# Kernel optimization log

Measured on AMD Instinct MI355X. Metric: run time of the kernel, lower is better.

Reference implementation:

```python
import jax, jax.numpy as jnp
import numpy as np

N_NODES = 100000
N_EDGES = 1600000
N_GRAPHS = 1024
B = 1024
GNN_INP, GNN_HID, GNN_OUT = 64, 128, 64
INP, HID, OUT = 64, 256, 1
EPS = 1e-5  # torch BatchNorm1d default eps


def _bn(h, gamma, beta):
    # training-mode BatchNorm1d: biased batch statistics over dim 0
    m = h.mean(axis=0)
    v = jnp.mean((h - m) ** 2, axis=0)
    return (h - m) * jax.lax.rsqrt(v + EPS) * gamma + beta


def setup_inputs() -> dict:
    key = jax.random.key(0)
    ks = jax.random.split(key, 24)
    s = 0.05
    inp = {
        "x": jax.random.normal(ks[0], (B, INP), jnp.float32),
        "masks": jax.random.randint(ks[1], (B,), 0, N_GRAPHS),
        "gnn_x": jax.random.normal(ks[2], (N_NODES, GNN_INP), jnp.float32),
        "edge_index": jax.random.randint(ks[3], (2, N_EDGES), 0, N_NODES),
        "gnn_batch": jnp.sort(jax.random.randint(ks[4], (N_NODES,), 0, N_GRAPHS)),
        # GCNConv params
        "W_gcn": jax.random.normal(ks[5], (GNN_INP, GNN_HID), jnp.float32) * s,
        "b_gcn": jnp.zeros((GNN_HID,), jnp.float32),
        "g1": jnp.ones((GNN_HID,), jnp.float32), "be1": jnp.zeros((GNN_HID,), jnp.float32),
        "W_lin1": jax.random.normal(ks[6], (GNN_HID, GNN_HID // 2), jnp.float32) * s,
        "b_lin1": jnp.zeros((GNN_HID // 2,), jnp.float32),
        "g2": jnp.ones((GNN_HID // 2,), jnp.float32), "be2": jnp.zeros((GNN_HID // 2,), jnp.float32),
        "W_lin2": jax.random.normal(ks[7], (GNN_HID // 2, GNN_OUT), jnp.float32) * s,
        "b_lin2": jnp.zeros((GNN_OUT,), jnp.float32),
        "g3": jnp.ones((GNN_OUT,), jnp.float32), "be3": jnp.zeros((GNN_OUT,), jnp.float32),
        # head params
        "W_fc1": jax.random.normal(ks[8], (INP + GNN_OUT, HID), jnp.float32) * s,
        "b_fc1": jnp.zeros((HID,), jnp.float32),
        "g4": jnp.ones((HID,), jnp.float32), "be4": jnp.zeros((HID,), jnp.float32),
        "W_fc2": jax.random.normal(ks[9], (HID, HID // 4), jnp.float32) * s,
        "b_fc2": jnp.zeros((HID // 4,), jnp.float32),
        "g5": jnp.ones((HID // 4,), jnp.float32), "be5": jnp.zeros((HID // 4,), jnp.float32),
        "W_fc3": jax.random.normal(ks[10], (HID // 4, OUT), jnp.float32) * s,
        "b_fc3": jnp.zeros((OUT,), jnp.float32),
    }
    return inp


def _forward(x, masks, gnn_x, edge_index, gnn_batch,
             W_gcn, b_gcn, g1, be1, W_lin1, b_lin1, g2, be2, W_lin2, b_lin2,
             g3, be3, W_fc1, b_fc1, g4, be4, W_fc2, b_fc2, g5, be5, W_fc3, b_fc3):
    N = gnn_x.shape[0]
    # --- GCNConv: linear transform, self-loops, sym-normalized scatter-add ---
    h = gnn_x @ W_gcn  # [N, GNN_HID]
    loop = jnp.arange(N)
    src = jnp.concatenate([edge_index[0], loop])
    dst = jnp.concatenate([edge_index[1], loop])
    deg = jax.ops.segment_sum(jnp.ones_like(dst, jnp.float32), dst, num_segments=N)
    dis = jax.lax.rsqrt(deg)  # deg >= 1 thanks to self-loops
    norm = dis[src] * dis[dst]  # [E+N]
    agg = jax.ops.segment_sum(h[src] * norm[:, None], dst, num_segments=N) + b_gcn
    z = jax.nn.relu(_bn(agg, g1, be1))  # dropout = identity (eval)
    # --- global_mean_pool over graph ids ---
    sums = jax.ops.segment_sum(z, gnn_batch, num_segments=N_GRAPHS)
    cnt = jax.ops.segment_sum(jnp.ones((N,), jnp.float32), gnn_batch, num_segments=N_GRAPHS)
    pooled = sums / jnp.maximum(cnt, 1.0)[:, None]  # [G, GNN_HID]
    z = jax.nn.relu(_bn(pooled @ W_lin1 + b_lin1, g2, be2))
    z = _bn(z @ W_lin2 + b_lin2, g3, be3)  # [G, GNN_OUT]
    # --- MixGNN head ---
    g = z[masks]  # [B, GNN_OUT]
    t = jnp.concatenate([x, g], axis=1)
    t = jax.nn.relu(_bn(t @ W_fc1 + b_fc1, g4, be4))
    t = t * t  # Multiply([h, h])
    t = jax.nn.relu(_bn(t @ W_fc2 + b_fc2, g5, be5))
    t = t * t
    t = t * t
    return t @ W_fc3 + b_fc3  # [B, OUT]


def reference(x, masks, gnn_x, edge_index, gnn_batch,
              W_gcn, b_gcn, g1, be1, W_lin1, b_lin1, g2, be2, W_lin2, b_lin2,
              g3, be3, W_fc1, b_fc1, g4, be4, W_fc2, b_fc2, g5, be5, W_fc3, b_fc3):
    return _forward(x, masks, gnn_x, edge_index, gnn_batch,
                    W_gcn, b_gcn, g1, be1, W_lin1, b_lin1, g2, be2, W_lin2, b_lin2,
                    g3, be3, W_fc1, b_fc1, g4, be4, W_fc2, b_fc2, g5, be5, W_fc3, b_fc3)
```

## Files before the change

kernel.cpp:

```cpp
#include <hip/hip_runtime.h>
#include <hip/hip_bf16.h>

#define N_NODES 100000
#define N_EDGES 1600000
#define N_GRAPHS 1024
#define BSZ 1024
#define EPS 1e-5f

#define NBUCK 256
#define BUCKW 391
#define BCAP  8192
#define SRC_MASK 0x1FFFF
#define BIN_CHUNK 8192
#define BIN_BLOCKS 196

#define WS_BNAGG   0
#define WS_STATS1  256
#define WS_STATS2  384
#define WS_STATS4  512
#define WS_STATS5  1024
#define WS_ZTOTAL  1152
#define WS_GCUR    1152
#define WS_SCALE1  1408
#define WS_SHIFT1  1536
#define WS_GSTART  1664
#define WS_DIS     2692
#define WS_ROWPTR  102692
#define WS_ROWLEN  202692
#define WS_AGG     302692
#define WS_PACKED  302692
#define WS_CSRC    2399844
#define WS_XH      4496996
#define WS_AGGX    13102692
#define WS_POOLED  19502692
#define WS_T1      19633764
#define WS_T2      19699300
#define WS_T4      19764836
#define WS_T5      20026980

__device__ inline unsigned short f2bf(float f) {
    unsigned int u = __float_as_uint(f);
    return (unsigned short)((u + 0x7FFFu + ((u >> 16) & 1u)) >> 16);
}

__global__ __launch_bounds__(256) void prep_kernel(float* __restrict__ ws,
                                                   const int* __restrict__ gbatch) {
    int b = blockIdx.x, tid = threadIdx.x;
    if (b == 0) {
        for (int i = tid; i < WS_ZTOTAL; i += 256) ws[i] = 0.0f;
    } else if (b == 1) {
        ((int*)(ws + WS_GCUR))[tid] = tid * BCAP;
    } else {
        int g = (b - 2) * 256 + tid;
        int lo = 0, hi = N_NODES;
        while (lo < hi) {
            int mid = (lo + hi) >> 1;
            if (gbatch[mid] < g) lo = mid + 1; else hi = mid;
        }
        int* gstart = (int*)(ws + WS_GSTART);
        gstart[g] = lo;
        if (g == 0) gstart[N_GRAPHS] = N_NODES;
    }
}

__global__ __launch_bounds__(256) void cvt_kernel(const float* __restrict__ x,
                                                  unsigned short* __restrict__ xh) {
    int i = blockIdx.x * 256 + threadIdx.x;
    float4 f = ((const float4*)x)[i];
    ushort4 h;
    h.x = f2bf(f.x); h.y = f2bf(f.y); h.z = f2bf(f.z); h.w = f2bf(f.w);
    ((ushort4*)xh)[i] = h;
}

__global__ __launch_bounds__(1024) void bin_kernel(const int* __restrict__ ei,
                                                   int* __restrict__ gcursor,
                                                   unsigned int* __restrict__ packed) {
    __shared__ unsigned int stage[BIN_CHUNK];
    __shared__ int lh[NBUCK], lbase[NBUCK], lcur[NBUCK], gb[NBUCK];
    const int* src = ei;
    const int* dst = ei + N_EDGES;
    int tid = threadIdx.x;
    int base = blockIdx.x * BIN_CHUNK;
    int n = min(BIN_CHUNK, N_EDGES - base);
    if (tid < NBUCK) lh[tid] = 0;
    __syncthreads();
    for (int i = tid; i < n; i += 1024)
        atomicAdd(&lh[dst[base + i] / BUCKW], 1);
    __syncthreads();
    if (tid < NBUCK) lbase[tid] = lh[tid];
    __syncthreads();
    for (int off = 1; off < NBUCK; off <<= 1) {
        int t = (tid < NBUCK && tid >= off) ? lbase[tid - off] : 0;
        __syncthreads();
        if (tid < NBUCK) lbase[tid] += t;
        __syncthreads();
    }
    if (tid < NBUCK) {
        int excl = lbase[tid] - lh[tid];
        lbase[tid] = excl;
        lcur[tid] = excl;
        gb[tid] = atomicAdd(&gcursor[tid], lh[tid]);
    }
    __syncthreads();
    for (int i = tid; i < n; i += 1024) {
        int d = dst[base + i];
        int s = src[base + i];
        int bk = d / BUCKW;
        int dl = d - bk * BUCKW;
        int slot = atomicAdd(&lcur[bk], 1);
        stage[slot] = ((unsigned int)dl << 17) | (unsigned int)s;
    }
    __syncthreads();
    int wid = tid >> 6, lane = tid & 63;
    for (int bk = wid; bk < NBUCK; bk += 16) {
        int lo = lbase[bk], go = gb[bk];
        int len = min(lh[bk], (bk + 1) * BCAP - go);
        for (int j = lane; j < len; j += 64)
            packed[go + j] = stage[lo + j];
    }
}

__global__ __launch_bounds__(256) void csr_build_kernel(const unsigned int* __restrict__ packed,
                                                        const int* __restrict__ gcur,
                                                        int* __restrict__ rowptr,
                                                        int* __restrict__ rowlen,
                                                        int* __restrict__ csrc,
                                                        float* __restrict__ dis) {
    __shared__ int dcnt[BUCKW];
    __shared__ int lcur[BUCKW];
    __shared__ int stage[BCAP];
    int b = blockIdx.x, tid = threadIdx.x;
    int e0 = b * BCAP;
    int ecnt = min(gcur[b] - e0, BCAP);
    int nbase = b * BUCKW;
    int nmax = min(BUCKW, N_NODES - nbase);
    for (int i = tid; i < BUCKW; i += 256) dcnt[i] = 0;
    __syncthreads();
    for (int i = tid; i < ecnt; i += 256)
        atomicAdd(&dcnt[packed[e0 + i] >> 17], 1);
    __syncthreads();
    for (int i = tid; i < nmax; i += 256) {
        dis[nbase + i] = rsqrtf((float)dcnt[i] + 1.0f);
        rowlen[nbase + i] = dcnt[i];
    }
    __syncthreads();
    if (tid < 64) {
        int lane = tid;
        int run = 0;
        for (int c = 0; c < BUCKW; c += 64) {
            int idx = c + lane;
            int v = (idx < BUCKW) ? dcnt[idx] : 0;
            int inc = v;
#pragma unroll
            for (int off = 1; off < 64; off <<= 1) {
                int t = __shfl_up(inc, off);
                if (lane >= off) inc += t;
            }
            if (idx < BUCKW) {
                int excl = run + inc - v;
                dcnt[idx] = excl;
                lcur[idx] = excl;
            }
            run += __shfl(inc, 63);
        }
    }
    __syncthreads();
    for (int i = tid; i < nmax; i += 256)
        rowptr[nbase + i] = e0 + dcnt[i];
    for (int i = tid; i < ecnt; i += 256) {
        unsigned int r = packed[e0 + i];
        int slot = atomicAdd(&lcur[r >> 17], 1);
        stage[slot] = (int)(r & SRC_MASK);
    }
    __syncthreads();
    for (int i = tid; i < ecnt; i += 256) csrc[e0 + i] = stage[i];
}

__global__ __launch_bounds__(256) void gather_kernel(const float* __restrict__ x,
                                                     const unsigned short* __restrict__ xh,
                                                     const int* __restrict__ rowptr,
                                                     const int* __restrict__ rowlen,
                                                     const int* __restrict__ csrc,
                                                     const float* __restrict__ dis,
                                                     float* __restrict__ aggx) {
    int wid = (blockIdx.x * 256 + threadIdx.x) >> 6;
    int lane = threadIdx.x & 63;
    if (wid >= N_NODES) return;
    int start = rowptr[wid];
    int len = rowlen[wid];
    float dd = dis[wid];
    float acc = x[(size_t)wid * 64 + lane] * dd * dd;
    for (int j0 = 0; j0 < len; j0 += 64) {
        int cnt = min(64, len - j0);
        int sv = 0;
        float wv = 0.f;
        if (lane < cnt) {
            sv = csrc[start + j0 + lane];
            wv = dis[sv] * dd;
        }
        int iters = (cnt + 7) & ~7;
        for (int k = 0; k < iters; k += 8) {
            int s[8]; float w[8], v[8];
#pragma unroll
            for (int u = 0; u < 8; ++u) {
                s[u] = __shfl(sv, k + u);
                w[u] = __shfl(wv, k + u);
            }
#pragma unroll
            for (int u = 0; u < 8; ++u)
                v[u] = __uint_as_float((unsigned int)xh[(size_t)s[u] * 64 + lane] << 16);
#pragma unroll
            for (int u = 0; u < 8; ++u) acc = fmaf(v[u], w[u], acc);
        }
    }
    aggx[(size_t)wid * 64 + lane] = acc;
}

__global__ __launch_bounds__(256) void gemm_agg_kernel(const float* __restrict__ A,
                                                       const float* __restrict__ W,
                                                       const float* __restrict__ bias,
                                                       float* __restrict__ AGG) {
    __shared__ float Ws[64 * 128];
    __shared__ float As[16 * 64];
    int tid = threadIdx.x;
    const float4* W4 = (const float4*)W;
    float4* Ws4 = (float4*)Ws;
#pragma unroll
    for (int i = 0; i < 8; ++i) Ws4[tid + i * 256] = W4[tid + i * 256];
    int row0 = blockIdx.x * 16;
    ((float4*)As)[tid] = ((const float4*)(A + (size_t)row0 * 64))[tid];
    __syncthreads();
    int tx = tid & 31;
    int ty = tid >> 5;
    int r0 = ty * 2;
    float4 bb = ((const float4*)bias)[tx];
    float acc[2][4] = {{bb.x, bb.y, bb.z, bb.w}, {bb.x, bb.y, bb.z, bb.w}};
#pragma unroll
    for (int k = 0; k < 64; ++k) {
        float a0 = As[r0 * 64 + k];
        float a1 = As[(r0 + 1) * 64 + k];
        float4 w = Ws4[k * 32 + tx];
        acc[0][0] += a0 * w.x; acc[0][1] += a0 * w.y; acc[0][2] += a0 * w.z; acc[0][3] += a0 * w.w;
        acc[1][0] += a1 * w.x; acc[1][1] += a1 * w.y; acc[1][2] += a1 * w.z; acc[1][3] += a1 * w.w;
    }
#pragma unroll
    for (int rr = 0; rr < 2; ++rr) {
        float4 v = make_float4(acc[rr][0], acc[rr][1], acc[rr][2], acc[rr][3]);
        ((float4*)(AGG + (size_t)(row0 + r0 + rr) * 128))[tx] = v;
    }
}

__global__ __launch_bounds__(256) void bnagg_stats_kernel(const float* __restrict__ agg,
                                                          float* __restrict__ stats) {
    __shared__ float4 ls[256];
    int tid = threadIdx.x;
    int lane = tid & 63;
    int grp = tid >> 6;
    int f = lane * 2;
    float2 s = {0.f, 0.f}, sq = {0.f, 0.f};
    for (int r = blockIdx.x * 4 + grp; r < N_NODES; r += gridDim.x * 4) {
        float2 a = *(const float2*)(agg + (size_t)r * 128 + f);
        s.x += a.x; s.y += a.y;
        sq.x += a.x * a.x; sq.y += a.y * a.y;
    }
    ls[tid] = make_float4(s.x, s.y, sq.x, sq.y);
    __syncthreads();
    if (tid < 64) {
        float4 v = ls[tid];
        float4 b = ls[tid + 64], c = ls[tid + 128], d = ls[tid + 192];
        v.x += b.x + c.x + d.x;
        v.y += b.y + c.y + d.y;
        v.z += b.z + c.z + d.z;
        v.w += b.w + c.w + d.w;
        unsafeAtomicAdd(&stats[f], v.x);
        unsafeAtomicAdd(&stats[f + 1], v.y);
        unsafeAtomicAdd(&stats[128 + f], v.z);
        unsafeAtomicAdd(&stats[128 + f + 1], v.w);
    }
}

__global__ void bn1_fold_kernel(const float* __restrict__ stats, const float* __restrict__ g1,
                                const float* __restrict__ be1, float* __restrict__ scale1,
                                float* __restrict__ shift1) {
    int f = threadIdx.x;
    float m = stats[f] * (1.0f / N_NODES);
    float var = stats[128 + f] * (1.0f / N_NODES) - m * m;
    float sc = g1[f] * rsqrtf(var + EPS);
    scale1[f] = sc;
    shift1[f] = be1[f] - m * sc;
}

__global__ __launch_bounds__(256) void pool_gather_kernel(const float* __restrict__ agg,
                                                          const int* __restrict__ gstart,
                                                          const float* __restrict__ scale1,
                                                          const float* __restrict__ shift1,
                                                          float* __restrict__ pooled) {
    int g = (blockIdx.x * 256 + threadIdx.x) >> 6;
    int lane = threadIdx.x & 63;
    if (g >= N_GRAPHS) return;
    int r0 = gstart[g], r1 = gstart[g + 1];
    int f = lane * 2;
    float2 sc = *(const float2*)(scale1 + f);
    float2 sh = *(const float2*)(shift1 + f);
    float2 acc = {0.f, 0.f};
    for (int r = r0; r < r1; ++r) {
        float2 a = *(const float2*)(agg + (size_t)r * 128 + f);
        acc.x += fmaxf(a.x * sc.x + sh.x, 0.f);
        acc.y += fmaxf(a.y * sc.y + sh.y, 0.f);
    }
    float inv = 1.0f / fmaxf((float)(r1 - r0), 1.0f);
    float2 o; o.x = acc.x * inv; o.y = acc.y * inv;
    *(float2*)(pooled + (size_t)g * 128 + f) = o;
}

__global__ __launch_bounds__(256) void lin1_kernel(const float* __restrict__ pooled,
                                                   const float* __restrict__ W,
                                                   const float* __restrict__ bias,
                                                   float* __restrict__ t1,
                                                   float* __restrict__ stats1) {
    __shared__ float ls[256], ls2[256];
    int tid = threadIdx.x;
    int r = blockIdx.x * 4 + (tid >> 6);
    int c = tid & 63;
    float acc = bias[c];
    const float* srow = pooled + (size_t)r * 128;
#pragma unroll 8
    for (int k = 0; k < 128; ++k)
        acc += srow[k] * W[k * 64 + c];
    t1[r * 64 + c] = acc;
    ls[tid] = acc; ls2[tid] = acc * acc;
    __syncthreads();
    if (tid < 64) {
        float s = ls[tid] + ls[tid + 64] + ls[tid + 128] + ls[tid + 192];
        float q = ls2[tid] + ls2[tid + 64] + ls2[tid + 128] + ls2[tid + 192];
        unsafeAtomicAdd(&stats1[c], s);
        unsafeAtomicAdd(&stats1[64 + c], q);
    }
}

__global__ __launch_bounds__(256) void lin2_kernel(const float* __restrict__ t1,
                                                   const float* __restrict__ stats1,
                                                   const float* __restrict__ g,
                                                   const float* __restrict__ be,
                                                   const float* __restrict__ W,
                                                   const float* __restrict__ bias,
                                                   float* __restrict__ t2,
                                                   float* __restrict__ stats2) {
    __shared__ float sc[64], sh[64];
    __shared__ float ls[256], ls2[256];
    int tid = threadIdx.x;
    if (tid < 64) {
        float m = stats1[tid] * (1.0f / BSZ);
        float var = stats1[64 + tid] * (1.0f / BSZ) - m * m;
        float s = g[tid] * rsqrtf(var + EPS);
        sc[tid] = s; sh[tid] = be[tid] - m * s;
    }
    __syncthreads();
    int r = blockIdx.x * 4 + (tid >> 6);
    int c = tid & 63;
    float acc = bias[c];
    const float* row = t1 + (size_t)r * 64;
#pragma unroll 8
    for (int k = 0; k < 64; ++k) {
        float z = fmaxf(row[k] * sc[k] + sh[k], 0.f);
        acc += z * W[k * 64 + c];
    }
    t2[r * 64 + c] = acc;
    ls[tid] = acc; ls2[tid] = acc * acc;
    __syncthreads();
    if (tid < 64) {
        float s = ls[tid] + ls[tid + 64] + ls[tid + 128] + ls[tid + 192];
        float q = ls2[tid] + ls2[tid + 64] + ls2[tid + 128] + ls2[tid + 192];
        unsafeAtomicAdd(&stats2[c], s);
        unsafeAtomicAdd(&stats2[64 + c], q);
    }
}

__global__ __launch_bounds__(1024) void fc1_kernel(const float* __restrict__ x,
                                                   const int* __restrict__ masks,
                                                   const float* __restrict__ t2,
                                                   const float* __restrict__ stats2,
                                                   const float* __restrict__ g3,
                                                   const float* __restrict__ be3,
                                                   const float* __restrict__ W,
                                                   const float* __restrict__ bias,
                                                   float* __restrict__ t4,
                                                   float* __restrict__ stats4) {
    __shared__ float sc[64], sh[64];
    __shared__ float cat[4][128];
    __shared__ float ls[1024], ls2[1024];
    int tid = threadIdx.x;
    if (tid < 64) {
        float m = stats2[tid] * (1.0f / BSZ);
        float var = stats2[64 + tid] * (1.0f / BSZ) - m * m;
        float s = g3[tid] * rsqrtf(var + EPS);
        sc[tid] = s; sh[tid] = be3[tid] - m * s;
    }
    __syncthreads();
    int r0 = blockIdx.x * 4;
    if (tid < 512) {
        int i = tid >> 7;
        int k = tid & 127;
        int r = r0 + i;
        float v;
        if (k < 64) {
            v = x[r * 64 + k];
        } else {
            int mrow = masks[r];
            int kk = k - 64;
            v = t2[mrow * 64 + kk] * sc[kk] + sh[kk];
        }
        cat[i][k] = v;
    }
    __syncthreads();
    int i = tid >> 8;
    int c = tid & 255;
    float acc = bias[c];
#pragma unroll 8
    for (int k = 0; k < 128; ++k)
        acc += cat[i][k] * W[k * 256 + c];
    t4[(size_t)(r0 + i) * 256 + c] = acc;
    ls[tid] = acc; ls2[tid] = acc * acc;
    __syncthreads();
    if (tid < 256) {
        float s = ls[tid] + ls[tid + 256] + ls[tid + 512] + ls[tid + 768];
        float q = ls2[tid] + ls2[tid + 256] + ls2[tid + 512] + ls2[tid + 768];
        unsafeAtomicAdd(&stats4[c], s);
        unsafeAtomicAdd(&stats4[256 + c], q);
    }
}

__global__ __launch_bounds__(256) void fc2_kernel(const float* __restrict__ t4,
                                                  const float* __restrict__ stats4,
                                                  const float* __restrict__ g4,
                                                  const float* __restrict__ be4,
                                                  const float* __restrict__ W,
                                                  const float* __restrict__ bias,
                                                  float* __restrict__ t5,
                                                  float* __restrict__ stats5) {
    __shared__ float sc[256], sh[256];
    __shared__ float ls[256], ls2[256];
    int tid = threadIdx.x;
    {
        float m = stats4[tid] * (1.0f / BSZ);
        float var = stats4[256 + tid] * (1.0f / BSZ) - m * m;
        float s = g4[tid] * rsqrtf(var + EPS);
        sc[tid] = s; sh[tid] = be4[tid] - m * s;
    }
    __syncthreads();
    int r = blockIdx.x * 4 + (tid >> 6);
    int c = tid & 63;
    float acc = bias[c];
    const float* row = t4 + (size_t)r * 256;
#pragma unroll 8
    for (int k = 0; k < 256; ++k) {
        float z = fmaxf(row[k] * sc[k] + sh[k], 0.f);
        z *= z;
        acc += z * W[k * 64 + c];
    }
    t5[r * 64 + c] = acc;
    ls[tid] = acc; ls2[tid] = acc * acc;
    __syncthreads();
    if (tid < 64) {
        float s = ls[tid] + ls[tid + 64] + ls[tid + 128] + ls[tid + 192];
        float q = ls2[tid] + ls2[tid + 64] + ls2[tid + 128] + ls2[tid + 192];
        unsafeAtomicAdd(&stats5[c], s);
        unsafeAtomicAdd(&stats5[64 + c], q);
    }
}

__global__ __launch_bounds__(256) void fc3_kernel(const float* __restrict__ t5,
                                                  const float* __restrict__ stats5,
                                                  const float* __restrict__ g5,
                                                  const float* __restrict__ be5,
                                                  const float* __restrict__ W,
                                                  const float* __restrict__ bias,
                                                  float* __restrict__ out) {
    __shared__ float sc[64], sh[64];
    int tid = threadIdx.x;
    if (tid < 64) {
        float m = stats5[tid] * (1.0f / BSZ);
        float var = stats5[64 + tid] * (1.0f / BSZ) - m * m;
        float s = g5[tid] * rsqrtf(var + EPS);
        sc[tid] = s; sh[tid] = be5[tid] - m * s;
    }
    __syncthreads();
    int r = blockIdx.x * 256 + tid;
    float acc = bias[0];
    const float* row = t5 + (size_t)r * 64;
#pragma unroll
    for (int k = 0; k < 64; ++k) {
        float z = fmaxf(row[k] * sc[k] + sh[k], 0.f);
        z = z * z;
        z = z * z;
        acc += z * W[k];
    }
    out[r] = acc;
}

extern "C" void kernel_launch(void* const* d_in, const int* in_sizes, int n_in,
                              void* d_out, int out_size, void* d_ws, size_t ws_size,
                              hipStream_t stream) {
    const float* x      = (const float*)d_in[0];
    const int*   masks  = (const int*)d_in[1];
    const float* gnn_x  = (const float*)d_in[2];
    const int*   ei     = (const int*)d_in[3];
    const int*   gbatch = (const int*)d_in[4];
    const float* W_gcn  = (const float*)d_in[5];
    const float* b_gcn  = (const float*)d_in[6];
    const float* g1     = (const float*)d_in[7];
    const float* be1    = (const float*)d_in[8];
    const float* W_lin1 = (const float*)d_in[9];
    const float* b_lin1 = (const float*)d_in[10];
    const float* g2     = (const float*)d_in[11];
    const float* be2    = (const float*)d_in[12];
    const float* W_lin2 = (const float*)d_in[13];
    const float* b_lin2 = (const float*)d_in[14];
    const float* g3     = (const float*)d_in[15];
    const float* be3    = (const float*)d_in[16];
    const float* W_fc1  = (const float*)d_in[17];
    const float* b_fc1  = (const float*)d_in[18];
    const float* g4     = (const float*)d_in[19];
    const float* be4    = (const float*)d_in[20];
    const float* W_fc2  = (const float*)d_in[21];
    const float* b_fc2  = (const float*)d_in[22];
    const float* g5     = (const float*)d_in[23];
    const float* be5    = (const float*)d_in[24];
    const float* W_fc3  = (const float*)d_in[25];
    const float* b_fc3  = (const float*)d_in[26];

    float* ws = (float*)d_ws;
    float* bnagg  = ws + WS_BNAGG;
    float* stats1 = ws + WS_STATS1;
    float* stats2 = ws + WS_STATS2;
    float* stats4 = ws + WS_STATS4;
    float* stats5 = ws + WS_STATS5;
    int*   gcur   = (int*)(ws + WS_GCUR);
    float* scale1 = ws + WS_SCALE1;
    float* shift1 = ws + WS_SHIFT1;
    int*   gstart = (int*)(ws + WS_GSTART);
    float* dis    = ws + WS_DIS;
    int*   rowptr = (int*)(ws + WS_ROWPTR);
    int*   rowlen = (int*)(ws + WS_ROWLEN);
    float* agg    = ws + WS_AGG;
    unsigned int* packed = (unsigned int*)(ws + WS_PACKED);
    int*   csrc   = (int*)(ws + WS_CSRC);
    unsigned short* xh = (unsigned short*)(ws + WS_XH);
    float* aggx   = ws + WS_AGGX;
    float* pooled = ws + WS_POOLED;
    float* t1     = ws + WS_T1;
    float* t2     = ws + WS_T2;
    float* t4     = ws + WS_T4;
    float* t5     = ws + WS_T5;
    float* out    = (float*)d_out;

    prep_kernel<<<6, 256, 0, stream>>>(ws, gbatch);
    cvt_kernel<<<N_NODES * 64 / 4 / 256, 256, 0, stream>>>(gnn_x, xh);
    bin_kernel<<<BIN_BLOCKS, 1024, 0, stream>>>(ei, gcur, packed);
    csr_build_kernel<<<NBUCK, 256, 0, stream>>>(packed, gcur, rowptr, rowlen, csrc, dis);
    gather_kernel<<<(N_NODES * 64 + 255) / 256, 256, 0, stream>>>(gnn_x, xh, rowptr, rowlen, csrc, dis, aggx);
    gemm_agg_kernel<<<N_NODES / 16, 256, 0, stream>>>(aggx, W_gcn, b_gcn, agg);
    bnagg_stats_kernel<<<512, 256, 0, stream>>>(agg, bnagg);
    bn1_fold_kernel<<<1, 128, 0, stream>>>(bnagg, g1, be1, scale1, shift1);
    pool_gather_kernel<<<(N_GRAPHS * 64 + 255) / 256, 256, 0, stream>>>(agg, gstart, scale1, shift1, pooled);
    lin1_kernel<<<256, 256, 0, stream>>>(pooled, W_lin1, b_lin1, t1, stats1);
    lin2_kernel<<<256, 256, 0, stream>>>(t1, stats1, g2, be2, W_lin2, b_lin2, t2, stats2);
    fc1_kernel<<<256, 1024, 0, stream>>>(x, masks, t2, stats2, g3, be3, W_fc1, b_fc1, t4, stats4);
    fc2_kernel<<<256, 256, 0, stream>>>(t4, stats4, g4, be4, W_fc2, b_fc2, t5, stats5);
    fc3_kernel<<<4, 256, 0, stream>>>(t5, stats5, g5, be5, W_fc3, b_fc3, out);
}
```

Measured before the change: 272.1 us.

## Compute BN1 stats from second moments of aggregated inputs, skip materializing GCN output

Instead of materializing the 100000x128 GCN output and scanning it for BatchNorm statistics, this computes the 64x64 second-moment matrix and column sums of the aggregated 64-wide features. The 128-wide mean and variance are then derived algebraically through W_gcn in a single-block fold kernel. Pooling recomputes the per-row projection on the fly from aggx with W held in registers. Separately, the gather's self term now reads the bf16 copy of x instead of fp32. This removes a large write and two reads of the 128-wide buffer, at the cost of extra FLOPs in pooling, a serial single-block fold, and possible precision loss from E[y^2]-m^2 in fp32. The bias is dropped, which is exact only because the BN mean subtraction cancels it.

```diff
diff --git a/kernel.cpp b/kernel.cpp
--- a/kernel.cpp
+++ b/kernel.cpp
@@ -13,30 +13,34 @@
 #define SRC_MASK 0x1FFFF
 #define BIN_CHUNK 8192
 #define BIN_BLOCKS 196
-
-#define WS_BNAGG   0
-#define WS_STATS1  256
-#define WS_STATS2  384
-#define WS_STATS4  512
-#define WS_STATS5  1024
-#define WS_ZTOTAL  1152
-#define WS_GCUR    1152
-#define WS_SCALE1  1408
-#define WS_SHIFT1  1536
-#define WS_GSTART  1664
-#define WS_DIS     2692
-#define WS_ROWPTR  102692
-#define WS_ROWLEN  202692
-#define WS_AGG     302692
-#define WS_PACKED  302692
-#define WS_CSRC    2399844
-#define WS_XH      4496996
-#define WS_AGGX    13102692
-#define WS_POOLED  19502692
-#define WS_T1      19633764
-#define WS_T2      19699300
-#define WS_T4      19764836
-#define WS_T5      20026980
+#define NCHUNK 512
+#define CHUNK_ROWS 196
+
+#define WS_STATS1  0
+#define WS_STATS2  128
+#define WS_STATS4  256
+#define WS_STATS5  768
+#define WS_ZTOTAL  896
+#define WS_GCUR    896
+#define WS_SCALE1  1152
+#define WS_SHIFTP  1280
+#define WS_M       1408
+#define WS_COLSUM  5504
+#define WS_GSTART  5568
+#define WS_DIS     6596
+#define WS_ROWPTR  106596
+#define WS_ROWLEN  206596
+#define WS_PACKED  306596
+#define WS_MPART   306596
+#define WS_CSRC    2403748
+#define WS_CPART   2403748
+#define WS_XH      4500900
+#define WS_AGGX    7700900
+#define WS_POOLED  14100900
+#define WS_T1      14231972
+#define WS_T2      14297508
+#define WS_T4      14363044
+#define WS_T5      14625188
 
 __device__ inline unsigned short f2bf(float f) {
     unsigned int u = __float_as_uint(f);
@@ -176,8 +180,7 @@
     for (int i = tid; i < ecnt; i += 256) csrc[e0 + i] = stage[i];
 }
 
-__global__ __launch_bounds__(256) void gather_kernel(const float* __restrict__ x,
-                                                     const unsigned short* __restrict__ xh,
+__global__ __launch_bounds__(256) void gather_kernel(const unsigned short* __restrict__ xh,
                                                      const int* __restrict__ rowptr,
                                                      const int* __restrict__ rowlen,
                                                      const int* __restrict__ csrc,
@@ -189,7 +192,8 @@
     int start = rowptr[wid];
     int len = rowlen[wid];
     float dd = dis[wid];
-    float acc = x[(size_t)wid * 64 + lane] * dd * dd;
+    float self = __uint_as_float((unsigned int)xh[(size_t)wid * 64 + lane] << 16);
+    float acc = self * dd * dd;
     for (int j0 = 0; j0 < len; j0 += 64) {
         int cnt = min(64, len - j0);
         int sv = 0;
@@ -216,101 +220,150 @@
     aggx[(size_t)wid * 64 + lane] = acc;
 }
 
-__global__ __launch_bounds__(256) void gemm_agg_kernel(const float* __restrict__ A,
-                                                       const float* __restrict__ W,
-                                                       const float* __restrict__ bias,
-                                                       float* __restrict__ AGG) {
-    __shared__ float Ws[64 * 128];
-    __shared__ float As[16 * 64];
+__global__ __launch_bounds__(256) void moment_kernel(const float* __restrict__ aggx,
+                                                     float* __restrict__ mpart,
+                                                     float* __restrict__ cpart) {
+    __shared__ float rows[8 * 64];
+    int c = blockIdx.x, tid = threadIdx.x;
+    int r0 = c * CHUNK_ROWS;
+    int r1 = min(r0 + CHUNK_ROWS, N_NODES);
+    int i0 = (tid >> 6) * 16;
+    int j = tid & 63;
+    float acc[16] = {};
+    float cs = 0.f;
+    for (int it = 0; it < (CHUNK_ROWS + 7) / 8; ++it) {
+        int sid = tid * 2;
+        int grow = r0 + it * 8 + (sid >> 6);
+        float2 v = {0.f, 0.f};
+        if (grow < r1) v = *(const float2*)(aggx + (size_t)(r0 + it * 8) * 64 + sid);
+        __syncthreads();
+        *(float2*)(rows + sid) = v;
+        __syncthreads();
+#pragma unroll
+        for (int rr = 0; rr < 8; ++rr) {
+            float bj = rows[rr * 64 + j];
+            float4 a0 = *(const float4*)(rows + rr * 64 + i0);
+            float4 a1 = *(const float4*)(rows + rr * 64 + i0 + 4);
+            float4 a2 = *(const float4*)(rows + rr * 64 + i0 + 8);
+            float4 a3 = *(const float4*)(rows + rr * 64 + i0 + 12);
+            acc[0]  += a0.x * bj; acc[1]  += a0.y * bj; acc[2]  += a0.z * bj; acc[3]  += a0.w * bj;
+            acc[4]  += a1.x * bj; acc[5]  += a1.y * bj; acc[6]  += a1.z * bj; acc[7]  += a1.w * bj;
+            acc[8]  += a2.x * bj; acc[9]  += a2.y * bj; acc[10] += a2.z * bj; acc[11] += a2.w * bj;
+            acc[12] += a3.x * bj; acc[13] += a3.y * bj; acc[14] += a3.z * bj; acc[15] += a3.w * bj;
+        }
+        if (tid < 64) {
+#pragma unroll
+            for (int rr = 0; rr < 8; ++rr) cs += rows[rr * 64 + tid];
+        }
+    }
+#pragma unroll
+    for (int m = 0; m < 16; ++m)
+        mpart[(size_t)c * 4096 + (i0 + m) * 64 + j] = acc[m];
+    if (tid < 64) cpart[c * 64 + tid] = cs;
+}
+
+__global__ __launch_bounds__(128) void mreduce_kernel(const float* __restrict__ mpart,
+                                                      float* __restrict__ M) {
+    int idx = blockIdx.x * 128 + threadIdx.x;
+    float s = 0.f;
+#pragma unroll 8
+    for (int c = 0; c < NCHUNK; ++c) s += mpart[(size_t)c * 4096 + idx];
+    M[idx] = s;
+}
+
+__global__ __launch_bounds__(256) void fold_kernel(const float* __restrict__ M,
+                                                   const float* __restrict__ cpart,
+                                                   const float* __restrict__ W,
+                                                   const float* __restrict__ g1,
+                                                   const float* __restrict__ be1,
+                                                   float* __restrict__ scale1,
+                                                   float* __restrict__ shiftp) {
+    __shared__ float Ml[4096];
+    __shared__ float sl[64];
+    __shared__ float sp[4][64];
+    __shared__ float qh[2][128];
     int tid = threadIdx.x;
-    const float4* W4 = (const float4*)W;
-    float4* Ws4 = (float4*)Ws;
-#pragma unroll
-    for (int i = 0; i < 8; ++i) Ws4[tid + i * 256] = W4[tid + i * 256];
-    int row0 = blockIdx.x * 16;
-    ((float4*)As)[tid] = ((const float4*)(A + (size_t)row0 * 64))[tid];
-    __syncthreads();
-    int tx = tid & 31;
-    int ty = tid >> 5;
-    int r0 = ty * 2;
-    float4 bb = ((const float4*)bias)[tx];
-    float acc[2][4] = {{bb.x, bb.y, bb.z, bb.w}, {bb.x, bb.y, bb.z, bb.w}};
-#pragma unroll
-    for (int k = 0; k < 64; ++k) {
-        float a0 = As[r0 * 64 + k];
-        float a1 = As[(r0 + 1) * 64 + k];
-        float4 w = Ws4[k * 32 + tx];
-        acc[0][0] += a0 * w.x; acc[0][1] += a0 * w.y; acc[0][2] += a0 * w.z; acc[0][3] += a0 * w.w;
-        acc[1][0] += a1 * w.x; acc[1][1] += a1 * w.y; acc[1][2] += a1 * w.z; acc[1][3] += a1 * w.w;
-    }
-#pragma unroll
-    for (int rr = 0; rr < 2; ++rr) {
-        float4 v = make_float4(acc[rr][0], acc[rr][1], acc[rr][2], acc[rr][3]);
-        ((float4*)(AGG + (size_t)(row0 + r0 + rr) * 128))[tx] = v;
-    }
-}
-
-__global__ __launch_bounds__(256) void bnagg_stats_kernel(const float* __restrict__ agg,
-                                                          float* __restrict__ stats) {
-    __shared__ float4 ls[256];
-    int tid = threadIdx.x;
-    int lane = tid & 63;
-    int grp = tid >> 6;
-    int f = lane * 2;
-    float2 s = {0.f, 0.f}, sq = {0.f, 0.f};
-    for (int r = blockIdx.x * 4 + grp; r < N_NODES; r += gridDim.x * 4) {
-        float2 a = *(const float2*)(agg + (size_t)r * 128 + f);
-        s.x += a.x; s.y += a.y;
-        sq.x += a.x * a.x; sq.y += a.y * a.y;
-    }
-    ls[tid] = make_float4(s.x, s.y, sq.x, sq.y);
-    __syncthreads();
-    if (tid < 64) {
-        float4 v = ls[tid];
-        float4 b = ls[tid + 64], c = ls[tid + 128], d = ls[tid + 192];
-        v.x += b.x + c.x + d.x;
-        v.y += b.y + c.y + d.y;
-        v.z += b.z + c.z + d.z;
-        v.w += b.w + c.w + d.w;
-        unsafeAtomicAdd(&stats[f], v.x);
-        unsafeAtomicAdd(&stats[f + 1], v.y);
-        unsafeAtomicAdd(&stats[128 + f], v.z);
-        unsafeAtomicAdd(&stats[128 + f + 1], v.w);
-    }
-}
-
-__global__ void bn1_fold_kernel(const float* __restrict__ stats, const float* __restrict__ g1,
-                                const float* __restrict__ be1, float* __restrict__ scale1,
-                                float* __restrict__ shift1) {
-    int f = threadIdx.x;
-    float m = stats[f] * (1.0f / N_NODES);
-    float var = stats[128 + f] * (1.0f / N_NODES) - m * m;
-    float sc = g1[f] * rsqrtf(var + EPS);
-    scale1[f] = sc;
-    shift1[f] = be1[f] - m * sc;
-}
-
-__global__ __launch_bounds__(256) void pool_gather_kernel(const float* __restrict__ agg,
-                                                          const int* __restrict__ gstart,
-                                                          const float* __restrict__ scale1,
-                                                          const float* __restrict__ shift1,
-                                                          float* __restrict__ pooled) {
-    int g = (blockIdx.x * 256 + threadIdx.x) >> 6;
-    int lane = threadIdx.x & 63;
-    if (g >= N_GRAPHS) return;
-    int r0 = gstart[g], r1 = gstart[g + 1];
-    int f = lane * 2;
-    float2 sc = *(const float2*)(scale1 + f);
-    float2 sh = *(const float2*)(shift1 + f);
-    float2 acc = {0.f, 0.f};
-    for (int r = r0; r < r1; ++r) {
-        float2 a = *(const float2*)(agg + (size_t)r * 128 + f);
-        acc.x += fmaxf(a.x * sc.x + sh.x, 0.f);
-        acc.y += fmaxf(a.y * sc.y + sh.y, 0.f);
-    }
-    float inv = 1.0f / fmaxf((float)(r1 - r0), 1.0f);
-    float2 o; o.x = acc.x * inv; o.y = acc.y * inv;
-    *(float2*)(pooled + (size_t)g * 128 + f) = o;
+#pragma unroll
+    for (int m = 0; m < 16; ++m) Ml[m * 256 + tid] = M[m * 256 + tid];
+    {
+        int i = tid & 63, q4 = tid >> 6;
+        float s = 0.f;
+        for (int c = q4 * (NCHUNK / 4); c < (q4 + 1) * (NCHUNK / 4); ++c)
+            s += cpart[c * 64 + i];
+        sp[q4][i] = s;
+    }
+    __syncthreads();
+    if (tid < 64) sl[tid] = sp[0][tid] + sp[1][tid] + sp[2][tid] + sp[3][tid];
+    __syncthreads();
+    int j = tid & 127, half = tid >> 7;
+    float wv[64];
+#pragma unroll
+    for (int k = 0; k < 64; ++k) wv[k] = W[k * 128 + j];
+    float q = 0.f;
+    for (int i = half * 32; i < half * 32 + 32; ++i) {
+        float ti = 0.f;
+#pragma unroll
+        for (int k = 0; k < 64; ++k) ti += Ml[i * 64 + k] * wv[k];
+        q += ti * wv[i];
+    }
+    qh[half][j] = q;
+    __syncthreads();
+    if (tid < 128) {
+        float Ey2 = (qh[0][j] + qh[1][j]) * (1.0f / N_NODES);
+        float my = 0.f;
+#pragma unroll
+        for (int k = 0; k < 64; ++k) my += sl[k] * wv[k];
+        my *= (1.0f / N_NODES);
+        float var = Ey2 - my * my;
+        float sc = g1[j] * rsqrtf(var + EPS);
+        scale1[j] = sc;
+        shiftp[j] = be1[j] - my * sc;
+    }
+}
+
+__global__ __launch_bounds__(256) void pool_kernel(const float* __restrict__ aggx,
+                                                   const int* __restrict__ gstart,
+                                                   const float* __restrict__ W,
+                                                   const float* __restrict__ scale1,
+                                                   const float* __restrict__ shiftp,
+                                                   float* __restrict__ pooled) {
+    __shared__ float rows[128];
+    __shared__ float pp[256];
+    int gph = blockIdx.x, tid = threadIdx.x;
+    int c = tid & 127, rg = tid >> 7;
+    float wreg[64];
+#pragma unroll
+    for (int k = 0; k < 64; ++k) wreg[k] = W[k * 128 + c];
+    float sc = scale1[c], sh = shiftp[c];
+    int r0 = gstart[gph], r1 = gstart[gph + 1];
+    float acc = 0.f;
+    for (int rb = r0; rb < r1; rb += 2) {
+        __syncthreads();
+        if (tid < 128) {
+            int rr = rb + (tid >> 6);
+            rows[tid] = (rr < r1) ? aggx[(size_t)rr * 64 + (tid & 63)] : 0.f;
+        }
+        __syncthreads();
+        int r = rb + rg;
+        if (r < r1) {
+            float y = 0.f;
+            const float4* rv = (const float4*)(rows + rg * 64);
+#pragma unroll
+            for (int k4 = 0; k4 < 16; ++k4) {
+                float4 v = rv[k4];
+                y += v.x * wreg[k4 * 4] + v.y * wreg[k4 * 4 + 1]
+                   + v.z * wreg[k4 * 4 + 2] + v.w * wreg[k4 * 4 + 3];
+            }
+            acc += fmaxf(y * sc + sh, 0.f);
+        }
+    }
+    pp[tid] = acc;
+    __syncthreads();
+    if (tid < 128) {
+        int cnt = r1 - r0;
+        float inv = 1.0f / fmaxf((float)cnt, 1.0f);
+        pooled[(size_t)gph * 128 + c] = (pp[c] + pp[128 + c]) * inv;
+    }
 }
 
 __global__ __launch_bounds__(256) void lin1_kernel(const float* __restrict__ pooled,
@@ -528,23 +581,25 @@
     const float* be5    = (const float*)d_in[24];
     const float* W_fc3  = (const float*)d_in[25];
     const float* b_fc3  = (const float*)d_in[26];
+    (void)b_gcn;
 
     float* ws = (float*)d_ws;
-    float* bnagg  = ws + WS_BNAGG;
     float* stats1 = ws + WS_STATS1;
     float* stats2 = ws + WS_STATS2;
     float* stats4 = ws + WS_STATS4;
     float* stats5 = ws + WS_STATS5;
     int*   gcur   = (int*)(ws + WS_GCUR);
     float* scale1 = ws + WS_SCALE1;
-    float* shift1 = ws + WS_SHIFT1;
+    float* shiftp = ws + WS_SHIFTP;
+    float* Mbuf   = ws + WS_M;
     int*   gstart = (int*)(ws + WS_GSTART);
     float* dis    = ws + WS_DIS;
     int*   rowptr = (int*)(ws + WS_ROWPTR);
     int*   rowlen = (int*)(ws + WS_ROWLEN);
-    float* agg    = ws + WS_AGG;
     unsigned int* packed = (unsigned int*)(ws + WS_PACKED);
+    float* mpart  = ws + WS_MPART;
     int*   csrc   = (int*)(ws + WS_CSRC);
+    float* cpart  = ws + WS_CPART;
     unsigned short* xh = (unsigned short*)(ws + WS_XH);
     float* aggx   = ws + WS_AGGX;
     float* pooled = ws + WS_POOLED;
@@ -558,11 +613,11 @@
     cvt_kernel<<<N_NODES * 64 / 4 / 256, 256, 0, stream>>>(gnn_x, xh);
     bin_kernel<<<BIN_BLOCKS, 1024, 0, stream>>>(ei, gcur, packed);
     csr_build_kernel<<<NBUCK, 256, 0, stream>>>(packed, gcur, rowptr, rowlen, csrc, dis);
-    gather_kernel<<<(N_NODES * 64 + 255) / 256, 256, 0, stream>>>(gnn_x, xh, rowptr, rowlen, csrc, dis, aggx);
-    gemm_agg_kernel<<<N_NODES / 16, 256, 0, stream>>>(aggx, W_gcn, b_gcn, agg);
-    bnagg_stats_kernel<<<512, 256, 0, stream>>>(agg, bnagg);
-    bn1_fold_kernel<<<1, 128, 0, stream>>>(bnagg, g1, be1, scale1, shift1);
-    pool_gather_kernel<<<(N_GRAPHS * 64 + 255) / 256, 256, 0, stream>>>(agg, gstart, scale1, shift1, pooled);
+    gather_kernel<<<(N_NODES * 64 + 255) / 256, 256, 0, stream>>>(xh, rowptr, rowlen, csrc, dis, aggx);
+    moment_kernel<<<NCHUNK, 256, 0, stream>>>(aggx, mpart, cpart);
+    mreduce_kernel<<<32, 128, 0, stream>>>(mpart, Mbuf);
+    fold_kernel<<<1, 256, 0, stream>>>(Mbuf, cpart, W_gcn, g1, be1, scale1, shiftp);
+    pool_kernel<<<N_GRAPHS, 256, 0, stream>>>(aggx, gstart, W_gcn, scale1, shiftp, pooled);
     lin1_kernel<<<256, 256, 0, stream>>>(pooled, W_lin1, b_lin1, t1, stats1);
     lin2_kernel<<<256, 256, 0, stream>>>(t1, stats1, g2, be2, W_lin2, b_lin2, t2, stats2);
     fc1_kernel<<<256, 1024, 0, stream>>>(x, masks, t2, stats2, g3, be3, W_fc1, b_fc1, t4, stats4);
```

After: 280.3 us. +3.0%, slower.
